# Kernel tuning notes

Measured on AMD Instinct MI355X. Metric: run time of the kernel, lower is better.

The kernel has to match this reference:

```python
import jax, jax.numpy as jnp
import numpy as np

NF, NS, GP = 5, 27, 4


def conv2d(x, w, b):
    y = jax.lax.conv_general_dilated(x, w, (1, 1), 'SAME',
                                     dimension_numbers=('NCHW', 'OIHW', 'NCHW'))
    return y + b[None, :, None, None]


def trilinear_sample(frames, tc, yc, xc):
    # frames: [b, nf, h, w]; tc/yc/xc: [b, NS, h, w] absolute (t, y, x) coords
    b, nf, h, w = frames.shape
    tc = jnp.clip(tc, 0.0, nf - 1.0)
    yc = jnp.clip(yc, 0.0, h - 1.0)
    xc = jnp.clip(xc, 0.0, w - 1.0)
    t0 = jnp.floor(tc); y0 = jnp.floor(yc); x0 = jnp.floor(xc)
    wt = tc - t0; wy = yc - y0; wx = xc - x0
    t0i = t0.astype(jnp.int32); y0i = y0.astype(jnp.int32); x0i = x0.astype(jnp.int32)
    t1i = jnp.minimum(t0i + 1, nf - 1)
    y1i = jnp.minimum(y0i + 1, h - 1)
    x1i = jnp.minimum(x0i + 1, w - 1)
    flat = frames.reshape(b, -1)

    def g(ti, yi, xi):
        idx = (ti * h + yi) * w + xi  # [b, NS, h, w]
        return jnp.take_along_axis(flat, idx.reshape(b, -1), axis=1).reshape(idx.shape)

    c000 = g(t0i, y0i, x0i); c001 = g(t0i, y0i, x1i)
    c010 = g(t0i, y1i, x0i); c011 = g(t0i, y1i, x1i)
    c100 = g(t1i, y0i, x0i); c101 = g(t1i, y0i, x1i)
    c110 = g(t1i, y1i, x0i); c111 = g(t1i, y1i, x1i)
    c00 = c000 * (1 - wx) + c001 * wx
    c01 = c010 * (1 - wx) + c011 * wx
    c10 = c100 * (1 - wx) + c101 * wx
    c11 = c110 * (1 - wx) + c111 * wx
    c0 = c00 * (1 - wy) + c01 * wy
    c1 = c10 * (1 - wy) + c11 * wy
    return c0 * (1 - wt) + c1 * wt


def samp(frames, offset):
    # offset: [b, NS*3, h, w] -> per-sample (dt, dy, dx)
    b, nf, h, w = frames.shape
    off = offset.reshape(b, NS, 3, h, w)
    grid = np.stack(np.meshgrid(np.arange(-1, 2), np.arange(-1, 2), np.arange(-1, 2),
                                indexing='ij'), -1).reshape(NS, 3).astype(np.float32)
    bt = jnp.asarray(grid[:, 0] + (NF - 1) // 2)[None, :, None, None]
    by = jnp.asarray(grid[:, 1])[None, :, None, None]
    bx = jnp.asarray(grid[:, 2])[None, :, None, None]
    yy = jnp.arange(h, dtype=frames.dtype)[None, None, :, None]
    xx = jnp.arange(w, dtype=frames.dtype)[None, None, None, :]
    tc = off[:, :, 0] + bt
    yc = off[:, :, 1] + by + yy
    xc = off[:, :, 2] + bx + xx
    return trilinear_sample(frames, tc, yc, xc)  # [b, NS, h, w]


def reference(frames, ow1, ob1, ow2, ob2, ow3, ob3, ww1, wb1, ww2, wb2, ww3, wb3):
    b, c, h, w = frames.shape
    # OffsetNet: two relu convs -> feat (128 ch), head -> offsets (NS*3 ch)
    f1 = jax.nn.relu(conv2d(frames, ow1, ob1))
    feat = jax.nn.relu(conv2d(f1, ow2, ob2))
    offset = conv2d(feat, ow3, ob3)
    samples = samp(frames, offset)  # [b, 27, h, w]
    cat = jnp.concatenate([frames, feat, samples], axis=1)  # [b, 160, h, w]
    # WeightsNet: three conv+relu
    wgt = jax.nn.relu(conv2d(cat, ww1, wb1))
    wgt = jax.nn.relu(conv2d(wgt, ww2, wb2))
    wgt = jax.nn.relu(conv2d(wgt, ww3, wb3))  # [b, 27, h, w]
    npg = NS // GP  # 6 -> only first GP*npg=24 samples used (torch.split + range(gp))
    s = samples[:, :GP * npg].reshape(b, GP, npg, h, w)
    wg = wgt[:, :GP * npg].reshape(b, GP, npg, h, w)
    gp_pred = GP * jnp.sum(s * wg, axis=2)  # [b, 4, h, w]
    avg = jnp.sum(gp_pred, axis=1, keepdims=True) / NS
    return gp_pred, avg


def setup_inputs() -> dict:
    key = jax.random.key(0)
    ks = jax.random.split(key, 8)
    B, H, W = 4, 512, 512

    def he(k, shape):
        fan_in = shape[1] * shape[2] * shape[3]
        return jax.random.normal(k, shape, jnp.float32) * np.sqrt(2.0 / fan_in)

    return {
        'frames': jax.random.uniform(ks[0], (B, NF, H, W), jnp.float32),
        'ow1': he(ks[1], (64, NF, 3, 3)), 'ob1': jnp.zeros((64,), jnp.float32),
        'ow2': he(ks[2], (128, 64, 3, 3)), 'ob2': jnp.zeros((128,), jnp.float32),
        'ow3': he(ks[3], (NS * 3, 128, 3, 3)) * 0.1, 'ob3': jnp.zeros((NS * 3,), jnp.float32),
        'ww1': he(ks[4], (64, NF + 128 + NS, 3, 3)), 'wb1': jnp.zeros((64,), jnp.float32),
        'ww2': he(ks[5], (64, 64, 3, 3)), 'wb2': jnp.zeros((64,), jnp.float32),
        'ww3': he(ks[6], (NS, 64, 3, 3)), 'wb3': jnp.zeros((NS,), jnp.float32),
    }
```

## Files before the change

### kernel.cpp

```cpp
#include <hip/hip_runtime.h>

#define HH 512
#define WW 512
#define HWP (HH * WW)

typedef unsigned short bf16_t;
typedef short bf16x8 __attribute__((ext_vector_type(8)));
typedef float f32x4 __attribute__((ext_vector_type(4)));
typedef unsigned short us4 __attribute__((ext_vector_type(4)));
typedef unsigned short us8 __attribute__((ext_vector_type(8)));

__device__ __forceinline__ float bf2f(bf16_t h) {
    union { unsigned int u; float f; } v; v.u = ((unsigned int)h) << 16; return v.f;
}
__device__ __forceinline__ bf16_t f2bf(float f) {
    union { float f; unsigned int u; } v; v.f = f;
    unsigned int r = (v.u + 0x7FFFu + ((v.u >> 16) & 1u)) >> 16;
    return (bf16_t)r;
}
__device__ __forceinline__ bf16x8 as_bf(us8 v) {
    union { us8 a; bf16x8 b; } u; u.a = v; return u.b;
}
__device__ __forceinline__ void gload16(const void* g, void* l) {
    __builtin_amdgcn_global_load_lds(
        (const __attribute__((address_space(1))) void*)g,
        (__attribute__((address_space(3))) void*)l, 16, 0, 0);
}

__global__ __launch_bounds__(256) void wprep_all(
    const float* __restrict__ w1, const float* __restrict__ w2,
    const float* __restrict__ w3, const float* __restrict__ w4,
    const float* __restrict__ w5, const float* __restrict__ w6,
    bf16_t* __restrict__ dst)
{
    int i = blockIdx.x * 256 + threadIdx.x;
    if (i >= 350720) return;
    if (i >= 350208) { dst[i] = 0; return; }
    const float* w; int Cout, Cin, COTF, KS, perm, base;
    if (i < 18432)       { w = w1; base = 0;      Cout = 64;  Cin = 5;   COTF = 4; KS = 1; perm = 0; }
    else if (i < 92160)  { w = w2; base = 18432;  Cout = 128; Cin = 64;  COTF = 8; KS = 2; perm = 0; }
    else if (i < 202752) { w = w3; base = 92160;  Cout = 81;  Cin = 128; COTF = 6; KS = 4; perm = 0; }
    else if (i < 294912) { w = w4; base = 202752; Cout = 64;  Cin = 160; COTF = 4; KS = 5; perm = 1; }
    else if (i < 331776) { w = w5; base = 294912; Cout = 64;  Cin = 64;  COTF = 4; KS = 2; perm = 0; }
    else                 { w = w6; base = 331776; Cout = 27;  Cin = 64;  COTF = 2; KS = 2; perm = 0; }
    int r = i - base;
    int j = r & 7;
    int lane = (r >> 3) & 63;
    int cot = (r >> 9) % COTF;
    int rest = r / (512 * COTF);
    int ks = rest % KS, tap = rest / KS;
    int col = lane & 15, hi = lane >> 4;
    int co = cot * 16 + col;
    int ci = ks * 32 + hi * 8 + j;
    float v = 0.f;
    if (co < Cout && ci < Cin) {
        int rci = ci;
        if (perm) rci = (ci < 128) ? ci + 5 : (ci < 133 ? ci - 128 : ci);
        v = w[((size_t)co * Cin + rci) * 9 + tap];
    }
    dst[i] = f2bf(v);
}

template<int COT, int KS>
__global__ __launch_bounds__(256, 2) void tconv(
    const bf16_t* __restrict__ in, size_t inImgStride,
    const bf16_t* __restrict__ wt, const float* __restrict__ bias,
    bf16_t* __restrict__ out, size_t outImgStride,
    int COTF, int Cout, int relu, const bf16_t* __restrict__ zp,
    int cinCh, const bf16_t* __restrict__ catp,
    float* __restrict__ fuseOut, int img0)
{
    __shared__ us8 buf[2][1584];
    const int tid = threadIdx.x;
    const int wave = tid >> 6, lane = tid & 63;
    const int col = lane & 15, hi = lane >> 4;
    const int img = blockIdx.y >> 7;
    const int yb0 = (blockIdx.y & 127) * 4;
    const int xb = blockIdx.x * 64;
    const int czbase = blockIdx.z * COT;
    const size_t slab = (size_t)HH * WW * 32;

    in += (size_t)img * inImgStride;
    out += (size_t)img * outImgStride;

    int gofs[7];
    bool ok[7];
#pragma unroll
    for (int k = 0; k < 7; ++k) {
        int u = tid + k * 256;
        if (u >= 1584) u = 1583;
        int row = (unsigned)u / 264u;
        int rem = u - row * 264;
        int px = rem >> 2, cs = rem & 3;
        int c = (cs - (px >> 1)) & 3;
        int yin = yb0 - 1 + row;
        int gx = xb - 1 + px;
        ok[k] = ((unsigned)yin < (unsigned)HH) && ((unsigned)gx < (unsigned)WW)
                && (c < cinCh);
        gofs[k] = ok[k] ? (int)(((size_t)yin * WW + gx) * 32 + c * 8) : 0;
    }

    auto STAGE = [&](int nb, int ks) {
#pragma unroll
        for (int k = 0; k < 7; ++k) {
            if (k == 6 && tid >= 48) continue;
            const bf16_t* g = ok[k] ? in + (size_t)ks * slab + gofs[k] : zp;
            gload16(g, (void*)&buf[nb][k * 256 + wave * 64]);
        }
    };

    f32x4 acc[4][COT] = {};
    bf16x8 a[9][COT];

    auto ALOAD = [&](int ks) {
#pragma unroll
        for (int t = 0; t < 9; ++t) {
#pragma unroll
            for (int c = 0; c < COT; ++c)
                a[t][c] = *(const bf16x8*)(wt
                    + (((size_t)t * KS + ks) * COTF + czbase + c) * 512 + lane * 8);
        }
    };

    auto COMPUTE = [&](int cb) {
#pragma unroll
        for (int dy = 0; dy < 3; ++dy) {
#pragma unroll
            for (int dx = 0; dx < 3; ++dx) {
                bf16x8 b[4];
#pragma unroll
                for (int pt = 0; pt < 4; ++pt) {
                    int X = pt * 16 + col + dx;
                    int unit = (wave + dy) * 264 + X * 4 + ((hi + (X >> 1)) & 3);
                    b[pt] = as_bf(buf[cb][unit]);
                }
#pragma unroll
                for (int c = 0; c < COT; ++c) {
#pragma unroll
                    for (int pt = 0; pt < 4; ++pt)
                        acc[pt][c] = __builtin_amdgcn_mfma_f32_16x16x32_bf16(
                            a[dy * 3 + dx][c], b[pt], acc[pt][c], 0, 0, 0);
                }
            }
        }
    };

    STAGE(0, 0);
    for (int ks = 0; ks < KS; ++ks) {
        ALOAD(ks);
        __builtin_amdgcn_sched_barrier(0);
        if (ks + 1 < KS) {
            STAGE((ks + 1) & 1, ks + 1);
            __builtin_amdgcn_sched_barrier(0);
            if constexpr (COT == 4)
                asm volatile("s_waitcnt vmcnt(42)" ::: "memory");
            else if constexpr (COT == 3)
                asm volatile("s_waitcnt vmcnt(33)" ::: "memory");
            else
                asm volatile("s_waitcnt vmcnt(24)" ::: "memory");
        } else {
            if constexpr (COT == 4)
                asm volatile("s_waitcnt vmcnt(36)" ::: "memory");
            else if constexpr (COT == 3)
                asm volatile("s_waitcnt vmcnt(27)" ::: "memory");
            else
                asm volatile("s_waitcnt vmcnt(18)" ::: "memory");
        }
        __builtin_amdgcn_sched_barrier(0);
        __builtin_amdgcn_s_barrier();
        __builtin_amdgcn_sched_barrier(0);
        COMPUTE(ks & 1);
        __builtin_amdgcn_s_barrier();
        __builtin_amdgcn_sched_barrier(0);
    }

    int y = yb0 + wave;

    if (fuseOut) {
        int gimg = img0 + img;
        const bf16_t* catim = catp + (size_t)img * inImgStride;
#pragma unroll
        for (int pt = 0; pt < 4; ++pt) {
            int x = xb + pt * 16 + col;
            const bf16_t* cp = catim + ((size_t)y * WW + x) * 32;
            float p[4] = {0.f, 0.f, 0.f, 0.f};
#pragma unroll
            for (int c = 0; c < COT; ++c) {
                int chb = (czbase + c) * 16 + hi * 4;
#pragma unroll
                for (int j = 0; j < 4; ++j) {
                    int ch = chb + j;
                    if (ch < 24) {
                        float wv = fmaxf(acc[pt][c][j] + bias[ch], 0.f);
                        p[ch / 6] += wv * bf2f(cp[5 + ch]);
                    }
                }
            }
#pragma unroll
            for (int g = 0; g < 4; ++g) {
                p[g] += __shfl_xor(p[g], 16);
                p[g] += __shfl_xor(p[g], 32);
            }
            if (hi == 0) {
                size_t pix = (size_t)y * WW + x;
                float tot = 0.f;
#pragma unroll
                for (int g = 0; g < 4; ++g) {
                    float gp = 4.f * p[g];
                    fuseOut[((size_t)gimg * 4 + g) * HWP + pix] = gp;
                    tot += gp;
                }
                fuseOut[(size_t)16 * HWP + (size_t)gimg * HWP + pix] = tot / 27.f;
            }
        }
        return;
    }

#pragma unroll
    for (int c = 0; c < COT; ++c) {
        int chbase = (czbase + c) * 16 + hi * 4;
        int slice = chbase >> 5, rem = chbase & 31;
        float bv[4];
#pragma unroll
        for (int j = 0; j < 4; ++j) {
            int co = chbase + j;
            bv[j] = (co < Cout) ? bias[co] : 0.f;
        }
#pragma unroll
        for (int pt = 0; pt < 4; ++pt) {
            int x = xb + pt * 16 + col;
            us4 o;
#pragma unroll
            for (int j = 0; j < 4; ++j) {
                float v = acc[pt][c][j] + bv[j];
                if (relu) v = fmaxf(v, 0.f);
                o[j] = f2bf(v);
            }
            *(us4*)(out + (((size_t)slice * HH + y) * WW + x) * 32 + rem) = o;
        }
    }
}

__global__ __launch_bounds__(256) void tr_fr32(
    const float* __restrict__ fr0, int img0,
    bf16_t* __restrict__ dst0, size_t stride)
{
    int img = blockIdx.y;
    int i = blockIdx.x * 256 + threadIdx.x;
    const float* fr = fr0 + (size_t)(img0 + img) * 5 * HWP;
    bf16_t* dst = dst0 + (size_t)img * stride;
    us8 v0 = {};
#pragma unroll
    for (int c = 0; c < 5; ++c) v0[c] = f2bf(fr[(size_t)c * HWP + i]);
    *(us8*)(dst + (size_t)i * 32) = v0;
}

__global__ __launch_bounds__(256, 4) void sample27f(
    const float* __restrict__ fr0, int img0,
    const bf16_t* __restrict__ of0, size_t stride,
    bf16_t* __restrict__ cat0)
{
    int img = blockIdx.y;
    int i = blockIdx.x * 256 + threadIdx.x;
    int y = i >> 9, x = i & 511;
    const float* f = fr0 + (size_t)(img0 + img) * 5 * HWP;
    const bf16_t* off = of0 + (size_t)img * stride;
    bf16_t* cat = cat0 + (size_t)img * stride;

    us8 ov[12];
#pragma unroll
    for (int sl = 0; sl < 3; ++sl)
#pragma unroll
        for (int c = 0; c < 4; ++c)
            ov[sl * 4 + c] = *(const us8*)(off
                + (((size_t)sl * HH + y) * WW + x) * 32 + c * 8);

    us8 outv[4];
#pragma unroll
    for (int c = 0; c < 5; ++c)
        outv[0][c] = f2bf(f[(size_t)c * HWP + i]);

#pragma unroll
    for (int s = 0; s < 27; ++s) {
        float dt  = bf2f((bf16_t)ov[(3 * s) >> 3][(3 * s) & 7]);
        float dyo = bf2f((bf16_t)ov[(3 * s + 1) >> 3][(3 * s + 1) & 7]);
        float dxo = bf2f((bf16_t)ov[(3 * s + 2) >> 3][(3 * s + 2) & 7]);
        float tc = dt + (float)(s / 9 + 1);
        float yc = dyo + (float)((s / 3) % 3 - 1) + (float)y;
        float xc = dxo + (float)(s % 3 - 1) + (float)x;
        tc = fminf(fmaxf(tc, 0.f), 4.f);
        yc = fminf(fmaxf(yc, 0.f), 511.f);
        xc = fminf(fmaxf(xc, 0.f), 511.f);
        float t0f = floorf(tc), y0f = floorf(yc), x0f = floorf(xc);
        float wt = tc - t0f, wy = yc - y0f, wx = xc - x0f;
        int t0 = (int)t0f, y0 = (int)y0f, x0 = (int)x0f;
        int t1 = min(t0 + 1, 4), y1 = min(y0 + 1, 511), x1 = min(x0 + 1, 511);
        float c000 = f[((size_t)t0 * HH + y0) * WW + x0];
        float c001 = f[((size_t)t0 * HH + y0) * WW + x1];
        float c010 = f[((size_t)t0 * HH + y1) * WW + x0];
        float c011 = f[((size_t)t0 * HH + y1) * WW + x1];
        float c100 = f[((size_t)t1 * HH + y0) * WW + x0];
        float c101 = f[((size_t)t1 * HH + y0) * WW + x1];
        float c110 = f[((size_t)t1 * HH + y1) * WW + x0];
        float c111 = f[((size_t)t1 * HH + y1) * WW + x1];
        float c00 = c000 * (1.f - wx) + c001 * wx;
        float c01 = c010 * (1.f - wx) + c011 * wx;
        float c10 = c100 * (1.f - wx) + c101 * wx;
        float c11 = c110 * (1.f - wx) + c111 * wx;
        float c0 = c00 * (1.f - wy) + c01 * wy;
        float c1 = c10 * (1.f - wy) + c11 * wy;
        int ch = 5 + s;
        outv[ch >> 3][ch & 7] = f2bf(c0 * (1.f - wt) + c1 * wt);
    }

    us8* o = (us8*)(cat + ((size_t)y * WW + x) * 32);
    o[0] = outv[0]; o[1] = outv[1]; o[2] = outv[2]; o[3] = outv[3];
}

static inline int cdiv(int a, int b) { return (a + b - 1) / b; }

extern "C" void kernel_launch(void* const* d_in, const int* in_sizes, int n_in,
                              void* d_out, int out_size, void* d_ws, size_t ws_size,
                              hipStream_t stream)
{
    const float* frames = (const float*)d_in[0];
    const float* ow1 = (const float*)d_in[1];
    const float* ob1 = (const float*)d_in[2];
    const float* ow2 = (const float*)d_in[3];
    const float* ob2 = (const float*)d_in[4];
    const float* ow3 = (const float*)d_in[5];
    const float* ob3 = (const float*)d_in[6];
    const float* ww1 = (const float*)d_in[7];
    const float* wb1 = (const float*)d_in[8];
    const float* ww2 = (const float*)d_in[9];
    const float* wb2 = (const float*)d_in[10];
    const float* ww3 = (const float*)d_in[11];
    const float* wb3 = (const float*)d_in[12];
    float* out = (float*)d_out;

    bf16_t* Wp = (bf16_t*)d_ws;
    const size_t wo1 = 0;
    const size_t wo2 = 18432;
    const size_t wo3 = 92160;
    const size_t wo4 = 202752;
    const size_t wo5 = 294912;
    const size_t wo6 = 331776;
    const size_t wzp = 350208;
    const size_t wtot = 350720;

    const size_t SLAB = (size_t)HH * WW * 32;
    const size_t PerImg = 7 * SLAB;

    size_t availElems = ws_size / sizeof(bf16_t);
    int NB = 1;
    if (wtot + 4 * PerImg <= availElems) NB = 4;
    else if (wtot + 2 * PerImg <= availElems) NB = 2;

    bf16_t* ZP = Wp + wzp;
    bf16_t* WS = Wp + wtot;

    wprep_all<<<cdiv(350720, 256), 256, 0, stream>>>(ow1, ow2, ow3, ww1, ww2, ww3, Wp);

    for (int s = 0; s < 4; s += NB) {
        int nb = (4 - s < NB) ? (4 - s) : NB;
        bf16_t* S0 = WS;
        bf16_t* S2 = WS + 2 * SLAB;
        bf16_t* S4 = WS + 4 * SLAB;
        bf16_t* S5 = WS + 5 * SLAB;
        bf16_t* S6 = WS + 6 * SLAB;

        tr_fr32<<<dim3(1024, nb), 256, 0, stream>>>(frames, s, S6, PerImg);
        tconv<4, 1><<<dim3(8, 128 * nb, 1), 256, 0, stream>>>(
            S6, PerImg, Wp + wo1, ob1, S4, PerImg, 4, 64, 1, ZP,
            1, nullptr, nullptr, 0);
        tconv<4, 2><<<dim3(8, 128 * nb, 2), 256, 0, stream>>>(
            S4, PerImg, Wp + wo2, ob2, S0, PerImg, 8, 128, 1, ZP,
            4, nullptr, nullptr, 0);
        tconv<3, 4><<<dim3(8, 128 * nb, 2), 256, 0, stream>>>(
            S0, PerImg, Wp + wo3, ob3, S4, PerImg, 6, 81, 0, ZP,
            4, nullptr, nullptr, 0);
        sample27f<<<dim3(1024, nb), 256, 0, stream>>>(frames, s, S4, PerImg, S4);
        tconv<4, 5><<<dim3(8, 128 * nb, 1), 256, 0, stream>>>(
            S0, PerImg, Wp + wo4, wb1, S5, PerImg, 4, 64, 1, ZP,
            4, nullptr, nullptr, 0);
        tconv<4, 2><<<dim3(8, 128 * nb, 1), 256, 0, stream>>>(
            S5, PerImg, Wp + wo5, wb2, S0, PerImg, 4, 64, 1, ZP,
            4, nullptr, nullptr, 0);
        tconv<2, 2><<<dim3(8, 128 * nb, 1), 256, 0, stream>>>(
            S0, PerImg, Wp + wo6, wb3, S2, PerImg, 2, 27, 1, ZP,
            4, S4, out, s);
    }
}
```

Baseline: 1.035 ms.

## Make conv blocks loop over row groups with cross-tile input prefetch

The implicit-GEMM conv kernel gains a YL template parameter, and each block now walks 8 consecutive 4-row tiles instead of one. The next tile's first input slab is staged into shared memory while the current tile's last K-slice is computed, so the global-load prologue is paid once per block. Grids shrink eightfold, toward about one wave of resident blocks, which cuts block launch and tail costs. In exchange there is less parallel slack for load balancing, and the wait is simplified to vmcnt(7), which forces the weight loads to finish before each compute step.

```diff
diff --git a/kernel.cpp b/kernel.cpp
--- a/kernel.cpp
+++ b/kernel.cpp
@@ -61,7 +61,7 @@
     dst[i] = f2bf(v);
 }
 
-template<int COT, int KS>
+template<int COT, int KS, int YL>
 __global__ __launch_bounds__(256, 2) void tconv(
     const bf16_t* __restrict__ in, size_t inImgStride,
     const bf16_t* __restrict__ wt, const float* __restrict__ bias,
@@ -74,8 +74,9 @@
     const int tid = threadIdx.x;
     const int wave = tid >> 6, lane = tid & 63;
     const int col = lane & 15, hi = lane >> 4;
-    const int img = blockIdx.y >> 7;
-    const int yb0 = (blockIdx.y & 127) * 4;
+    constexpr int YG = 128 / YL;
+    const int img = blockIdx.y / YG;
+    const int ygrp = blockIdx.y % YG;
     const int xb = blockIdx.x * 64;
     const int czbase = blockIdx.z * COT;
     const size_t slab = (size_t)HH * WW * 32;
@@ -83,8 +84,8 @@
     in += (size_t)img * inImgStride;
     out += (size_t)img * outImgStride;
 
-    int gofs[7];
-    bool ok[7];
+    int rowk[7], xpart[7];
+    bool okx[7];
 #pragma unroll
     for (int k = 0; k < 7; ++k) {
         int u = tid + k * 256;
@@ -93,12 +94,22 @@
         int rem = u - row * 264;
         int px = rem >> 2, cs = rem & 3;
         int c = (cs - (px >> 1)) & 3;
-        int yin = yb0 - 1 + row;
         int gx = xb - 1 + px;
-        ok[k] = ((unsigned)yin < (unsigned)HH) && ((unsigned)gx < (unsigned)WW)
-                && (c < cinCh);
-        gofs[k] = ok[k] ? (int)(((size_t)yin * WW + gx) * 32 + c * 8) : 0;
+        okx[k] = ((unsigned)gx < (unsigned)WW) && (c < cinCh);
+        rowk[k] = row;
+        xpart[k] = gx * 32 + c * 8;
     }
+
+    int gofs[7];
+    bool ok[7];
+    auto SETG = [&](int yb) {
+#pragma unroll
+        for (int k = 0; k < 7; ++k) {
+            int yin = yb - 1 + rowk[k];
+            ok[k] = okx[k] && ((unsigned)yin < (unsigned)HH);
+            gofs[k] = yin * (WW * 32) + xpart[k];
+        }
+    };
 
     auto STAGE = [&](int nb, int ks) {
 #pragma unroll
@@ -145,99 +156,102 @@
         }
     };
 
+    const int yb0 = ygrp * (4 * YL);
+    SETG(yb0);
     STAGE(0, 0);
-    for (int ks = 0; ks < KS; ++ks) {
-        ALOAD(ks);
-        __builtin_amdgcn_sched_barrier(0);
-        if (ks + 1 < KS) {
-            STAGE((ks + 1) & 1, ks + 1);
+    int cur = 0;
+
+#pragma unroll 1
+    for (int yi = 0; yi < YL; ++yi) {
+        const int yb = yb0 + yi * 4;
+        for (int ks = 0; ks < KS; ++ks) {
+            ALOAD(ks);
             __builtin_amdgcn_sched_barrier(0);
-            if constexpr (COT == 4)
-                asm volatile("s_waitcnt vmcnt(42)" ::: "memory");
-            else if constexpr (COT == 3)
-                asm volatile("s_waitcnt vmcnt(33)" ::: "memory");
-            else
-                asm volatile("s_waitcnt vmcnt(24)" ::: "memory");
+            if (!((yi == YL - 1) && (ks == KS - 1))) {
+                if (ks == KS - 1) SETG(yb + 4);
+                STAGE(cur ^ 1, (ks == KS - 1) ? 0 : ks + 1);
+                __builtin_amdgcn_sched_barrier(0);
+                asm volatile("s_waitcnt vmcnt(7)" ::: "memory");
+            } else {
+                asm volatile("s_waitcnt vmcnt(0)" ::: "memory");
+            }
+            __builtin_amdgcn_sched_barrier(0);
+            __builtin_amdgcn_s_barrier();
+            __builtin_amdgcn_sched_barrier(0);
+            COMPUTE(cur);
+            __builtin_amdgcn_s_barrier();
+            __builtin_amdgcn_sched_barrier(0);
+            cur ^= 1;
+        }
+
+        int y = yb + wave;
+        if (fuseOut) {
+            int gimg = img0 + img;
+            const bf16_t* catim = catp + (size_t)img * inImgStride;
+#pragma unroll
+            for (int pt = 0; pt < 4; ++pt) {
+                int x = xb + pt * 16 + col;
+                const bf16_t* cp = catim + ((size_t)y * WW + x) * 32;
+                float p[4] = {0.f, 0.f, 0.f, 0.f};
+#pragma unroll
+                for (int c = 0; c < COT; ++c) {
+                    int chb = (czbase + c) * 16 + hi * 4;
+#pragma unroll
+                    for (int j = 0; j < 4; ++j) {
+                        int ch = chb + j;
+                        if (ch < 24) {
+                            float wv = fmaxf(acc[pt][c][j] + bias[ch], 0.f);
+                            p[ch / 6] += wv * bf2f(cp[5 + ch]);
+                        }
+                    }
+                }
+#pragma unroll
+                for (int g = 0; g < 4; ++g) {
+                    p[g] += __shfl_xor(p[g], 16);
+                    p[g] += __shfl_xor(p[g], 32);
+                }
+                if (hi == 0) {
+                    size_t pix = (size_t)y * WW + x;
+                    float tot = 0.f;
+#pragma unroll
+                    for (int g = 0; g < 4; ++g) {
+                        float gp = 4.f * p[g];
+                        fuseOut[((size_t)gimg * 4 + g) * HWP + pix] = gp;
+                        tot += gp;
+                    }
+                    fuseOut[(size_t)16 * HWP + (size_t)gimg * HWP + pix] = tot / 27.f;
+                }
+            }
         } else {
-            if constexpr (COT == 4)
-                asm volatile("s_waitcnt vmcnt(36)" ::: "memory");
-            else if constexpr (COT == 3)
-                asm volatile("s_waitcnt vmcnt(27)" ::: "memory");
-            else
-                asm volatile("s_waitcnt vmcnt(18)" ::: "memory");
-        }
-        __builtin_amdgcn_sched_barrier(0);
-        __builtin_amdgcn_s_barrier();
-        __builtin_amdgcn_sched_barrier(0);
-        COMPUTE(ks & 1);
-        __builtin_amdgcn_s_barrier();
-        __builtin_amdgcn_sched_barrier(0);
-    }
-
-    int y = yb0 + wave;
-
-    if (fuseOut) {
-        int gimg = img0 + img;
-        const bf16_t* catim = catp + (size_t)img * inImgStride;
-#pragma unroll
-        for (int pt = 0; pt < 4; ++pt) {
-            int x = xb + pt * 16 + col;
-            const bf16_t* cp = catim + ((size_t)y * WW + x) * 32;
-            float p[4] = {0.f, 0.f, 0.f, 0.f};
 #pragma unroll
             for (int c = 0; c < COT; ++c) {
-                int chb = (czbase + c) * 16 + hi * 4;
+                int chbase = (czbase + c) * 16 + hi * 4;
+                int slice = chbase >> 5, rem = chbase & 31;
+                float bv[4];
 #pragma unroll
                 for (int j = 0; j < 4; ++j) {
-                    int ch = chb + j;
-                    if (ch < 24) {
-                        float wv = fmaxf(acc[pt][c][j] + bias[ch], 0.f);
-                        p[ch / 6] += wv * bf2f(cp[5 + ch]);
+                    int co = chbase + j;
+                    bv[j] = (co < Cout) ? bias[co] : 0.f;
+                }
+#pragma unroll
+                for (int pt = 0; pt < 4; ++pt) {
+                    int x = xb + pt * 16 + col;
+                    us4 o;
+#pragma unroll
+                    for (int j = 0; j < 4; ++j) {
+                        float v = acc[pt][c][j] + bv[j];
+                        if (relu) v = fmaxf(v, 0.f);
+                        o[j] = f2bf(v);
                     }
+                    *(us4*)(out + (((size_t)slice * HH + y) * WW + x) * 32 + rem) = o;
                 }
             }
-#pragma unroll
-            for (int g = 0; g < 4; ++g) {
-                p[g] += __shfl_xor(p[g], 16);
-                p[g] += __shfl_xor(p[g], 32);
-            }
-            if (hi == 0) {
-                size_t pix = (size_t)y * WW + x;
-                float tot = 0.f;
-#pragma unroll
-                for (int g = 0; g < 4; ++g) {
-                    float gp = 4.f * p[g];
-                    fuseOut[((size_t)gimg * 4 + g) * HWP + pix] = gp;
-                    tot += gp;
-                }
-                fuseOut[(size_t)16 * HWP + (size_t)gimg * HWP + pix] = tot / 27.f;
-            }
-        }
-        return;
-    }
-
-#pragma unroll
-    for (int c = 0; c < COT; ++c) {
-        int chbase = (czbase + c) * 16 + hi * 4;
-        int slice = chbase >> 5, rem = chbase & 31;
-        float bv[4];
-#pragma unroll
-        for (int j = 0; j < 4; ++j) {
-            int co = chbase + j;
-            bv[j] = (co < Cout) ? bias[co] : 0.f;
-        }
-#pragma unroll
-        for (int pt = 0; pt < 4; ++pt) {
-            int x = xb + pt * 16 + col;
-            us4 o;
-#pragma unroll
-            for (int j = 0; j < 4; ++j) {
-                float v = acc[pt][c][j] + bv[j];
-                if (relu) v = fmaxf(v, 0.f);
-                o[j] = f2bf(v);
-            }
-            *(us4*)(out + (((size_t)slice * HH + y) * WW + x) * 32 + rem) = o;
-        }
+        }
+#pragma unroll
+        for (int pt = 0; pt < 4; ++pt)
+#pragma unroll
+            for (int c = 0; c < COT; ++c)
+                acc[pt][c] = f32x4{};
     }
 }
 
@@ -370,23 +384,23 @@
         bf16_t* S6 = WS + 6 * SLAB;
 
         tr_fr32<<<dim3(1024, nb), 256, 0, stream>>>(frames, s, S6, PerImg);
-        tconv<4, 1><<<dim3(8, 128 * nb, 1), 256, 0, stream>>>(
+        tconv<4, 1, 8><<<dim3(8, 16 * nb, 1), 256, 0, stream>>>(
             S6, PerImg, Wp + wo1, ob1, S4, PerImg, 4, 64, 1, ZP,
             1, nullptr, nullptr, 0);
-        tconv<4, 2><<<dim3(8, 128 * nb, 2), 256, 0, stream>>>(
+        tconv<4, 2, 8><<<dim3(8, 16 * nb, 2), 256, 0, stream>>>(
             S4, PerImg, Wp + wo2, ob2, S0, PerImg, 8, 128, 1, ZP,
             4, nullptr, nullptr, 0);
-        tconv<3, 4><<<dim3(8, 128 * nb, 2), 256, 0, stream>>>(
+        tconv<3, 4, 8><<<dim3(8, 16 * nb, 2), 256, 0, stream>>>(
             S0, PerImg, Wp + wo3, ob3, S4, PerImg, 6, 81, 0, ZP,
             4, nullptr, nullptr, 0);
         sample27f<<<dim3(1024, nb), 256, 0, stream>>>(frames, s, S4, PerImg, S4);
-        tconv<4, 5><<<dim3(8, 128 * nb, 1), 256, 0, stream>>>(
+        tconv<4, 5, 8><<<dim3(8, 16 * nb, 1), 256, 0, stream>>>(
             S0, PerImg, Wp + wo4, wb1, S5, PerImg, 4, 64, 1, ZP,
             4, nullptr, nullptr, 0);
-        tconv<4, 2><<<dim3(8, 128 * nb, 1), 256, 0, stream>>>(
+        tconv<4, 2, 8><<<dim3(8, 16 * nb, 1), 256, 0, stream>>>(
             S5, PerImg, Wp + wo5, wb2, S0, PerImg, 4, 64, 1, ZP,
             4, nullptr, nullptr, 0);
-        tconv<2, 2><<<dim3(8, 128 * nb, 1), 256, 0, stream>>>(
+        tconv<2, 2, 8><<<dim3(8, 16 * nb, 1), 256, 0, stream>>>(
             S0, PerImg, Wp + wo6, wb3, S2, PerImg, 2, 27, 1, ZP,
             4, S4, out, s);
     }
```

After: 2.090 ms. 102% more time.
